# Kernel tuning notes

Hardware: AMD Instinct MI355X
Metric: run time of the kernel (lower is better)

The kernel has to match this reference:

```python
import jax, jax.numpy as jnp
import numpy as np

DIM_TIME = 100
NUM_HEAD = 8
DIM_OUT = 256
LN_EPS = 1e-5

# fixed (non-trainable) TimeEncode frequencies: 1 / 10**linspace(0, 9, dim)
_TIME_W = jnp.asarray((1.0 / 10 ** np.linspace(0, 9, DIM_TIME, dtype=np.float32)))


def setup_inputs() -> dict:
    key = jax.random.key(0)
    ks = jax.random.split(key, 16)
    D, E, S = 25000, 500000, 525000
    dn, de = 128, 128
    def lin(k, out_d, in_d):
        return jax.random.normal(k, (out_d, in_d), jnp.float32) * (1.0 / np.sqrt(in_d))
    return {
        "h": jax.random.normal(ks[0], (S, dn), jnp.float32),
        "f": jax.random.normal(ks[1], (E, de), jnp.float32),
        "dt": jax.random.uniform(ks[2], (E,), jnp.float32) * 1000.0,
        "Wq_lin": lin(ks[3], DIM_OUT, dn + DIM_TIME),
        "bq_lin": jnp.zeros((DIM_OUT,), jnp.float32),
        "Wkv_lin": lin(ks[4], DIM_OUT, dn + de + DIM_TIME),
        "bkv_lin": jnp.zeros((DIM_OUT,), jnp.float32),
        "Wq": lin(ks[5], DIM_OUT, DIM_OUT),
        "bq": jnp.zeros((DIM_OUT,), jnp.float32),
        "Wk": lin(ks[6], DIM_OUT, DIM_OUT),
        "bk": jnp.zeros((DIM_OUT,), jnp.float32),
        "Wv": lin(ks[7], DIM_OUT, DIM_OUT),
        "bv": jnp.zeros((DIM_OUT,), jnp.float32),
        "ln_g": jnp.ones((DIM_OUT,), jnp.float32),
        "ln_b": jnp.zeros((DIM_OUT,), jnp.float32),
        "dst": jax.random.randint(ks[8], (E,), 0, D, jnp.int64 if jax.config.jax_enable_x64 else jnp.int32),
    }


def reference(h, f, dt, Wq_lin, bq_lin, Wkv_lin, bkv_lin, Wq, bq, Wk, bk, Wv, bv, ln_g, ln_b, dst):
    E = dst.shape[0]
    D = h.shape[0] - E          # num_dst_nodes; src node D+i is the source of edge i
    H = NUM_HEAD
    dh = DIM_OUT // H

    # TimeEncode (frozen, no grad in original): cos(w * t + 0)
    time_feat = jax.lax.stop_gradient(jnp.cos(dt[:, None] * _TIME_W[None, :]))      # [E, Dt]
    zero_time_feat = jnp.ones((D, DIM_TIME), h.dtype)                               # cos(0) = 1

    # Q from dst nodes; K/V from src-neighbor nodes + edge feat + time feat
    Q_ori = jnp.concatenate([h[:D], zero_time_feat], axis=1) @ Wq_lin.T + bq_lin    # [D, dout]
    K_ori = jnp.concatenate([h[D:], f, time_feat], axis=1) @ Wkv_lin.T + bkv_lin    # [E, dout]

    # augmented edge set: E real edges + D self-loops (dst attends to itself)
    Qfull = jnp.concatenate([Q_ori[dst], Q_ori], axis=0)                            # [E+D, dout]
    KVfull = jnp.concatenate([K_ori, Q_ori], axis=0)                                # [E+D, dout]

    Qh = (Qfull @ Wq.T + bq).reshape(-1, H, dh)
    Kh = (KVfull @ Wk.T + bk).reshape(-1, H, dh)
    Vh = (KVfull @ Wv.T + bv).reshape(-1, H, dh)

    scores = jax.nn.leaky_relu(jnp.sum(Qh * Kh, axis=2), negative_slope=0.2)        # [E+D, H]

    dst_all = jnp.concatenate([dst, jnp.arange(D, dtype=dst.dtype)], axis=0)        # [E+D]

    # segment (edge) softmax over destination nodes; every dst has a self-loop
    seg_max = jnp.full((D, H), -jnp.inf, scores.dtype).at[dst_all].max(scores)
    ex = jnp.exp(scores - seg_max[dst_all])
    seg_sum = jnp.zeros((D, H), scores.dtype).at[dst_all].add(ex)
    att = ex / seg_sum[dst_all]                                                     # [E+D, H]

    # weighted scatter-sum aggregation (copy_u/sum over the augmented block)
    Vw = (Vh * att[:, :, None]).reshape(-1, DIM_OUT)                                # [E+D, dout]
    agg = jnp.zeros((D, DIM_OUT), h.dtype).at[dst_all].add(Vw)                      # [D, dout]

    rst = jax.nn.relu(agg)                                                          # dropout = identity (eval)
    mu = jnp.mean(rst, axis=-1, keepdims=True)
    var = jnp.mean((rst - mu) ** 2, axis=-1, keepdims=True)
    return (rst - mu) * jax.lax.rsqrt(var + LN_EPS) * ln_g + ln_b
```

## Files before the change

kernel.cpp:

```cpp
#include <hip/hip_runtime.h>
#include <cstdint>
#include <cstddef>


typedef _Float16 f16_t;
typedef _Float16 f16x8 __attribute__((ext_vector_type(8)));
typedef _Float16 f16x4 __attribute__((ext_vector_type(4)));
typedef float    f32x4 __attribute__((ext_vector_type(4)));

#define MFMA16(a, b, c) __builtin_amdgcn_mfma_f32_16x16x32_f16(a, b, c, 0, 0, 0)

#define BARRIER()                                         \
  do {                                                    \
    asm volatile("s_waitcnt lgkmcnt(0)" ::: "memory");    \
    __builtin_amdgcn_sched_barrier(0);                    \
    __builtin_amdgcn_s_barrier();                         \
    __builtin_amdgcn_sched_barrier(0);                    \
  } while (0)

static __device__ __forceinline__ f32x4 zero4() {
  f32x4 v; v[0] = 0.f; v[1] = 0.f; v[2] = 0.f; v[3] = 0.f; return v;
}

#define TIMEW_LOG2 (-0.30199346317157837f)

__global__ void k_prep(const float* __restrict__ wq_lin,
                       const float* __restrict__ bq_lin,
                       const float* __restrict__ wq,
                       const float* __restrict__ wk,
                       const float* __restrict__ wv,
                       f16_t* __restrict__ wq1,
                       f16_t* __restrict__ w3,
                       float* __restrict__ bqe) {
  int i = blockIdx.x * 256 + threadIdx.x;
  if (i < 32768) {
    int o = i >> 7, k = i & 127;
    wq1[i] = (f16_t)wq_lin[o * 228 + k];
  } else if (i < 229376) {
    int j = i - 32768;
    int r = j >> 8, k = j & 255;
    const float* src = (r < 256) ? wq : ((r < 512) ? wk : wv);
    w3[j] = (f16_t)src[(r & 255) * 256 + k];
  } else if (i < 229632) {
    int o = i - 229376;
    float s = bq_lin[o];
    for (int j = 0; j < 100; ++j) s += wq_lin[o * 228 + 128 + j];
    bqe[o] = s;
  }
}

__global__ __launch_bounds__(384) void k_wcomp(
    const float* __restrict__ wkv_lin, const float* __restrict__ bkv,
    const float* __restrict__ wk, const float* __restrict__ bk,
    const float* __restrict__ wv, const float* __restrict__ bv,
    f16_t* __restrict__ weffp, float* __restrict__ beff) {
  __shared__ float wrow[256];
  const int oc = blockIdx.x;
  const float* src = (oc < 256) ? (wk + (size_t)oc * 256)
                                : (wv + (size_t)(oc - 256) * 256);
  const int t = threadIdx.x;
  if (t < 256) wrow[t] = src[t];
  __syncthreads();

  float acc = 0.f;
  if (t < 356) {
#pragma unroll 4
    for (int m = 0; m < 256; ++m) acc += wrow[m] * wkv_lin[(size_t)m * 356 + t];
  }
  int kc = t >> 5, g = (t >> 3) & 3, j = t & 7;
  weffp[(size_t)kc * 16384 + g * 4096 + oc * 8 + j] = (f16_t)acc;

  if (t == 0) {
    float b = (oc < 256) ? bk[oc] : bv[oc - 256];
    for (int m = 0; m < 256; ++m) b += wrow[m] * bkv[m];
    beff[oc] = b;
  }
}

__global__ void k_hist(const int* __restrict__ dst, int* __restrict__ rs, int E) {
  int e = blockIdx.x * 256 + threadIdx.x;
  if (e < E) atomicAdd(&rs[dst[e] + 1], 1);
}

__global__ void k_scan(int* __restrict__ rs, int* __restrict__ cur, int D) {
  __shared__ int sd[1024];
  __shared__ int srun;
  const int t = threadIdx.x;
  if (t == 0) srun = 0;
  __syncthreads();
  for (int base = 0; base < D; base += 1024) {
    const int i = base + t;
    int c = (i < D) ? rs[i + 1] : 0;
    sd[t] = c;
    __syncthreads();
    for (int off = 1; off < 1024; off <<= 1) {
      int v = (t >= off) ? sd[t - off] : 0;
      __syncthreads();
      sd[t] += v;
      __syncthreads();
    }
    const int incl = sd[t];
    const int run = srun;
    __syncthreads();
    if (i < D) {
      cur[i] = run + incl - c;
      rs[i + 1] = run + incl;
    }
    if (t == 1023) srun = run + sd[1023];
    __syncthreads();
  }
}

__global__ void k_scatter(const int* __restrict__ dst, int* __restrict__ cur,
                          int* __restrict__ csr, int* __restrict__ dstc, int E) {
  int e = blockIdx.x * 256 + threadIdx.x;
  if (e < E) {
    int d = dst[e];
    int pos = atomicAdd(&cur[d], 1);
    csr[pos] = e;
    dstc[pos] = d;
  }
}

__global__ void k_sentinel(float* __restrict__ o, int n) {
  int i = blockIdx.x * 256 + threadIdx.x;
  if (i < n) o[i] = 1e30f;
}

__global__ __launch_bounds__(512) void k_q(
    const float* __restrict__ h, const float* __restrict__ bqe,
    const float* __restrict__ bq, const float* __restrict__ bk,
    const float* __restrict__ bv, const f16_t* __restrict__ wq1,
    const f16_t* __restrict__ w3, float* __restrict__ qhd,
    f16_t* __restrict__ khs, f16_t* __restrict__ vhs, int D) {
  __shared__ f16_t sm[64 * 256];
  f16_t* xs = sm;
  f16_t* ks = sm;
  const int tid = threadIdx.x;
  const int dbase = blockIdx.x * 64;

  {
    const int r = tid >> 3, q = tid & 7;
    const int dd = min(dbase + r, D - 1);
    const int sw = r & 7;
    const float* p = h + (size_t)dd * 128 + q * 16;
#pragma unroll
    for (int u = 0; u < 2; ++u) {
      float4 v0 = *(const float4*)(p + u * 8);
      float4 v1 = *(const float4*)(p + u * 8 + 4);
      f16x8 w8;
      w8[0] = (f16_t)v0.x; w8[1] = (f16_t)v0.y; w8[2] = (f16_t)v0.z; w8[3] = (f16_t)v0.w;
      w8[4] = (f16_t)v1.x; w8[5] = (f16_t)v1.y; w8[6] = (f16_t)v1.z; w8[7] = (f16_t)v1.w;
      *(f16x8*)&xs[r * 128 + (((2 * q + u) ^ sw) << 3)] = w8;
    }
  }
  __syncthreads();

  const int lane = tid & 63;
  const int wv_ = tid >> 6;
  const int m16 = lane & 15;
  const int g = lane >> 4;

  f32x4 acc1[4][2];
#pragma unroll
  for (int mt = 0; mt < 4; ++mt)
#pragma unroll
    for (int nt = 0; nt < 2; ++nt) acc1[mt][nt] = zero4();

#pragma unroll
  for (int kt = 0; kt < 4; ++kt) {
    f16x8 a[4];
#pragma unroll
    for (int mt = 0; mt < 4; ++mt) {
      int row = mt * 16 + m16;
      a[mt] = *(const f16x8*)&xs[row * 128 + ((((kt << 2) + g) ^ (row & 7)) << 3)];
    }
#pragma unroll
    for (int nt = 0; nt < 2; ++nt) {
      int col = wv_ * 32 + nt * 16 + m16;
      f16x8 b = *(const f16x8*)&wq1[(size_t)col * 128 + (kt << 5) + (g << 3)];
#pragma unroll
      for (int mt = 0; mt < 4; ++mt) acc1[mt][nt] = MFMA16(a[mt], b, acc1[mt][nt]);
    }
  }
  __syncthreads();

#pragma unroll
  for (int nt = 0; nt < 2; ++nt) {
    int col = wv_ * 32 + nt * 16 + m16;
    float bias = bqe[col];
#pragma unroll
    for (int mt = 0; mt < 4; ++mt)
#pragma unroll
      for (int j = 0; j < 4; ++j) {
        int row = mt * 16 + (g << 2) + j;
        ks[row * 256 + ((((col >> 3) ^ (row & 7)) << 3)) + (col & 7)] =
            (f16_t)(acc1[mt][nt][j] + bias);
      }
  }
  __syncthreads();

#pragma unroll
  for (int p = 0; p < 3; ++p) {
    const f16_t* wsec = w3 + ((size_t)p << 16);
    const float* bsec = (p == 0) ? bq : ((p == 1) ? bk : bv);
    f32x4 acc[4][2];
#pragma unroll
    for (int mt = 0; mt < 4; ++mt)
#pragma unroll
      for (int nt = 0; nt < 2; ++nt) acc[mt][nt] = zero4();
#pragma unroll
    for (int kt = 0; kt < 8; ++kt) {
      f16x8 a[4];
#pragma unroll
      for (int mt = 0; mt < 4; ++mt) {
        int row = mt * 16 + m16;
        a[mt] = *(const f16x8*)&ks[row * 256 + ((((kt << 2) + g) ^ (row & 7)) << 3)];
      }
#pragma unroll
      for (int nt = 0; nt < 2; ++nt) {
        int col = wv_ * 32 + nt * 16 + m16;
        f16x8 b = *(const f16x8*)&wsec[(size_t)col * 256 + (kt << 5) + (g << 3)];
#pragma unroll
        for (int mt = 0; mt < 4; ++mt) acc[mt][nt] = MFMA16(a[mt], b, acc[mt][nt]);
      }
    }
#pragma unroll
    for (int nt = 0; nt < 2; ++nt) {
      int col = wv_ * 32 + nt * 16 + m16;
      float bias = bsec[col];
#pragma unroll
      for (int mt = 0; mt < 4; ++mt)
#pragma unroll
        for (int j = 0; j < 4; ++j) {
          int row = mt * 16 + (g << 2) + j;
          int dd = dbase + row;
          if (dd < D) {
            float val = acc[mt][nt][j] + bias;
            if (p == 0)
              qhd[(size_t)dd * 256 + col] = val;
            else if (p == 1)
              khs[(size_t)dd * 256 + col] = (f16_t)val;
            else
              vhs[(size_t)dd * 256 + col] = (f16_t)val;
          }
        }
    }
  }
}

__global__ __launch_bounds__(512, 4) void k_kv(
    const float* __restrict__ h, const float* __restrict__ f,
    const float* __restrict__ dt, const f16_t* __restrict__ weffp,
    const float* __restrict__ beff, const int* __restrict__ csr,
    const int* __restrict__ dstc, const float* __restrict__ qhd,
    float* __restrict__ att, f16_t* __restrict__ vhg, int D, int E) {
  __shared__ __align__(16) unsigned char smem[40960];

  const int tid = threadIdx.x;
  const int pbase = blockIdx.x * 64;
  const int row = tid >> 3, q = tid & 7;
  const int lane = tid & 63, wn = tid >> 6;
  const int m16 = lane & 15, g = lane >> 4;

  const int pclamp = min(pbase + row, E - 1);
  const int ec = csr[pclamp];
  const float dtv = dt[ec];
  const float* hrow = h + (size_t)(D + ec) * 128 + q * 4;
  const float* frow = f + (size_t)ec * 128 + q * 4;

  auto stageA = [&](int buf, int sub, float4 v) {
    f16x4 w;
    w[0] = (f16_t)v.x; w[1] = (f16_t)v.y; w[2] = (f16_t)v.z; w[3] = (f16_t)v.w;
    *(f16x4*)(smem + buf * 20480 + sub * 5120 + row * 80 + q * 8) = w;
  };
  const f16_t* wb = weffp + (size_t)g * 4096 + ((size_t)(wn * 64 + m16) << 3);
  auto gldB = [&](int kc, f16x8* d) {
    const f16_t* pB = wb + (size_t)kc * 16384;
#pragma unroll
    for (int n = 0; n < 4; ++n) d[n] = *(const f16x8*)(pB + n * 128);
  };

  f32x4 acc[4][4];
#pragma unroll
  for (int mt = 0; mt < 4; ++mt)
#pragma unroll
    for (int n = 0; n < 4; ++n) acc[mt][n] = zero4();

  auto doChunk = [&](int kc, const f16x8* bbuf) {
    const unsigned char* Ac =
        smem + (((kc >> 2) == 1) ? 20480 : 0) + (kc & 3) * 5120;
#pragma unroll
    for (int mt = 0; mt < 4; ++mt) {
      f16x8 afr = *(const f16x8*)(Ac + (mt * 16 + m16) * 80 + g * 16);
#pragma unroll
      for (int n = 0; n < 4; ++n) acc[mt][n] = MFMA16(afr, bbuf[n], acc[mt][n]);
    }
  };

  float4 hv[4], fv[4];
#pragma unroll
  for (int s = 0; s < 4; ++s) hv[s] = *(const float4*)(hrow + s * 32);
#pragma unroll
  for (int s = 0; s < 4; ++s) fv[s] = *(const float4*)(frow + s * 32);
#pragma unroll
  for (int s = 0; s < 4; ++s) stageA(0, s, hv[s]);
#pragma unroll
  for (int s = 0; s < 4; ++s) stageA(1, s, fv[s]);
  BARRIER();

  f16x8 bb0[4], bb1[4];
  gldB(0, bb0);
  gldB(1, bb1); doChunk(0, bb0);
  gldB(2, bb0); doChunk(1, bb1);
  gldB(3, bb1); doChunk(2, bb0);
  gldB(4, bb0); doChunk(3, bb1);
  BARRIER();

#pragma unroll
  for (int s = 0; s < 4; ++s) {
    float4 a;
#pragma unroll
    for (int j = 0; j < 4; ++j) {
      int cc = s * 32 + q * 4 + j;
      ((float*)&a)[j] =
          (cc < 100) ? __cosf(dtv * exp2f(TIMEW_LOG2 * (float)cc)) : 0.f;
    }
    stageA(0, s, a);
  }
  gldB(5, bb1); doChunk(4, bb0);
  gldB(6, bb0); doChunk(5, bb1);
  gldB(7, bb1); doChunk(6, bb0);
  gldB(8, bb0); doChunk(7, bb1);
  BARRIER();

  gldB(9, bb1);  doChunk(8, bb0);
  gldB(10, bb0); doChunk(9, bb1);
  gldB(11, bb1); doChunk(10, bb0);
  doChunk(11, bb1);
  BARRIER();

  f16_t* ep = (f16_t*)smem;

  if (wn < 4) {
#pragma unroll
    for (int n = 0; n < 4; ++n) {
      const int c256 = wn * 64 + n * 16 + m16;
      const float bias = beff[c256];
#pragma unroll
      for (int mt = 0; mt < 4; ++mt)
#pragma unroll
        for (int j = 0; j < 4; ++j) {
          const int r2 = mt * 16 + (g << 2) + j;
          ep[r2 * 264 + c256] = (f16_t)(acc[mt][n][j] + bias);
        }
    }
  }
  BARRIER();

  {
    const int r2 = tid >> 3, hp = tid & 7;
    const int p2 = pbase + r2;
    if (p2 < E) {
      const int de = dstc[p2];
      const float* qp = qhd + (size_t)de * 256 + hp * 32;
      const f16_t* kp = ep + r2 * 264 + hp * 32;
      float s = 0.f;
#pragma unroll
      for (int jj = 0; jj < 32; jj += 4) {
        float4 qv = *(const float4*)(qp + jj);
        f16x4 kv = *(const f16x4*)(kp + jj);
        s += qv.x * (float)kv[0] + qv.y * (float)kv[1] +
             qv.z * (float)kv[2] + qv.w * (float)kv[3];
      }
      s = (s > 0.f) ? s : 0.2f * s;
      att[(size_t)p2 * 8 + hp] = __expf(s);
    }
  }
  BARRIER();

  if (wn >= 4) {
#pragma unroll
    for (int n = 0; n < 4; ++n) {
      const int c256 = (wn - 4) * 64 + n * 16 + m16;
      const float bias = beff[256 + c256];
#pragma unroll
      for (int mt = 0; mt < 4; ++mt)
#pragma unroll
        for (int j = 0; j < 4; ++j) {
          const int r2 = mt * 16 + (g << 2) + j;
          ep[r2 * 264 + c256] = (f16_t)(acc[mt][n][j] + bias);
        }
    }
  }
  BARRIER();

#pragma unroll
  for (int sweep = 0; sweep < 4; ++sweep) {
    const int flat = sweep * 4096 + tid * 8;
    const int r2 = flat >> 8, cc = flat & 255;
    const int p2 = pbase + r2;
    if (p2 < E) {
      f16x8 v = *(const f16x8*)&ep[r2 * 264 + cc];
      *(f16x8*)&vhg[(size_t)p2 * 256 + cc] = v;
    }
  }
}

__global__ __launch_bounds__(256) void k_agg(
    const float* __restrict__ qhd, const f16_t* __restrict__ khs,
    const f16_t* __restrict__ vhs, const float* __restrict__ att,
    const f16_t* __restrict__ vhg, const int* __restrict__ rs,
    const float* __restrict__ lng, const float* __restrict__ lnb,
    float* __restrict__ out, int D) {
  const int lane = threadIdx.x & 63;
  const int d = blockIdx.x * 4 + (threadIdx.x >> 6);
  if (d >= D) return;
  const int c0 = lane * 4;
  const int hd = lane >> 3;

  float den, a0, a1, a2, a3;
  {
    float4 qv = *(const float4*)(qhd + (size_t)d * 256 + c0);
    f16x4 ku = *(const f16x4*)(khs + (size_t)d * 256 + c0);
    f16x4 vu = *(const f16x4*)(vhs + (size_t)d * 256 + c0);
    float s = qv.x * (float)ku[0] + qv.y * (float)ku[1] +
              qv.z * (float)ku[2] + qv.w * (float)ku[3];
    s += __shfl_xor(s, 1); s += __shfl_xor(s, 2); s += __shfl_xor(s, 4);
    s = (s > 0.f) ? s : 0.2f * s;
    float ee = __expf(s);
    den = ee;
    a0 = ee * (float)vu[0]; a1 = ee * (float)vu[1];
    a2 = ee * (float)vu[2]; a3 = ee * (float)vu[3];
  }

  const int beg = rs[d], end = rs[d + 1];
  float ea0 = 0.f, ea1 = 0.f, ea2 = 0.f, ea3 = 0.f;
  float eb0 = 0.f, eb1 = 0.f, eb2 = 0.f, eb3 = 0.f;
  f16x4 va0 = {}, va1 = {}, va2 = {}, va3 = {};
  f16x4 vb0 = {}, vb1 = {}, vb2 = {}, vb3 = {};

#define LDQ(i, ee, vv)                                          \
  if ((i) < end) {                                              \
    ee = att[(size_t)(i) * 8 + hd];                             \
    vv = *(const f16x4*)(vhg + (size_t)(i) * 256 + c0);         \
  }
#define ACC(ee, vv)                                             \
  do {                                                          \
    den += ee;                                                  \
    a0 = fmaf(ee, (float)vv[0], a0);                            \
    a1 = fmaf(ee, (float)vv[1], a1);                            \
    a2 = fmaf(ee, (float)vv[2], a2);                            \
    a3 = fmaf(ee, (float)vv[3], a3);                            \
  } while (0)

  LDQ(beg + 0, ea0, va0);
  LDQ(beg + 1, ea1, va1);
  LDQ(beg + 2, ea2, va2);
  LDQ(beg + 3, ea3, va3);
  for (int idx = beg; idx < end; idx += 4) {
    LDQ(idx + 4, eb0, vb0);
    LDQ(idx + 5, eb1, vb1);
    LDQ(idx + 6, eb2, vb2);
    LDQ(idx + 7, eb3, vb3);
    ACC(ea0, va0);
    if (idx + 1 < end) ACC(ea1, va1);
    if (idx + 2 < end) ACC(ea2, va2);
    if (idx + 3 < end) ACC(ea3, va3);
    ea0 = eb0; va0 = vb0;
    ea1 = eb1; va1 = vb1;
    ea2 = eb2; va2 = vb2;
    ea3 = eb3; va3 = vb3;
  }
#undef LDQ
#undef ACC

  float x0 = fmaxf(a0 / den, 0.f), x1 = fmaxf(a1 / den, 0.f);
  float x2 = fmaxf(a2 / den, 0.f), x3 = fmaxf(a3 / den, 0.f);

  float s1 = x0 + x1 + x2 + x3;
#pragma unroll
  for (int m = 1; m < 64; m <<= 1) s1 += __shfl_xor(s1, m);
  float mu = s1 * (1.f / 256.f);
  float d0 = x0 - mu, d1 = x1 - mu, d2 = x2 - mu, d3 = x3 - mu;
  float s2 = d0 * d0 + d1 * d1 + d2 * d2 + d3 * d3;
#pragma unroll
  for (int m = 1; m < 64; m <<= 1) s2 += __shfl_xor(s2, m);
  float rstd = rsqrtf(s2 * (1.f / 256.f) + 1e-5f);

  float4 gg = *(const float4*)(lng + c0);
  float4 bb = *(const float4*)(lnb + c0);
  float4 o;
  o.x = d0 * rstd * gg.x + bb.x;
  o.y = d1 * rstd * gg.y + bb.y;
  o.z = d2 * rstd * gg.z + bb.z;
  o.w = d3 * rstd * gg.w + bb.w;
  *(float4*)(out + (size_t)d * 256 + c0) = o;
}

extern "C" void kernel_launch(void* const* d_in, const int* in_sizes, int n_in,
                              void* d_out, int out_size, void* d_ws,
                              size_t ws_size, hipStream_t stream) {
  const float* h       = (const float*)d_in[0];
  const float* f       = (const float*)d_in[1];
  const float* dt      = (const float*)d_in[2];
  const float* wq_lin  = (const float*)d_in[3];
  const float* bq_lin  = (const float*)d_in[4];
  const float* wkv_lin = (const float*)d_in[5];
  const float* bkv_lin = (const float*)d_in[6];
  const float* wq      = (const float*)d_in[7];
  const float* bq      = (const float*)d_in[8];
  const float* wk      = (const float*)d_in[9];
  const float* bk      = (const float*)d_in[10];
  const float* wv      = (const float*)d_in[11];
  const float* bv      = (const float*)d_in[12];
  const float* lng     = (const float*)d_in[13];
  const float* lnb     = (const float*)d_in[14];
  const int*   dst     = (const int*)d_in[15];

  const int S = in_sizes[0] / 128;
  const int E = in_sizes[2];
  const int D = S - E;
  float* out = (float*)d_out;

  char* p = (char*)d_ws;
  size_t off = 0;
  auto take = [&](size_t bytes) -> char* {
    char* r = p + off;
    off += (bytes + 255) & ~(size_t)255;
    return r;
  };
  f16_t* wq1   = (f16_t*)take((size_t)32768 * 2);
  f16_t* w3    = (f16_t*)take((size_t)196608 * 2);
  float* bqe   = (float*)take((size_t)256 * 4);
  f16_t* weffp = (f16_t*)take((size_t)196608 * 2);
  float* beff  = (float*)take((size_t)512 * 4);
  float* qhd   = (float*)take((size_t)D * 256 * 4);
  f16_t* khs   = (f16_t*)take((size_t)D * 256 * 2);
  f16_t* vhs   = (f16_t*)take((size_t)D * 256 * 2);
  float* att   = (float*)take((size_t)E * 8 * 4);
  f16_t* vhg   = (f16_t*)take((size_t)E * 256 * 2);
  int*   rs    = (int*)  take((size_t)(D + 1) * 4);
  int*   cur   = (int*)  take((size_t)D * 4);
  int*   csr   = (int*)  take((size_t)E * 4);
  int*   dstc  = (int*)  take((size_t)E * 4);

  if (off > ws_size) {
    k_sentinel<<<(out_size + 255) / 256, 256, 0, stream>>>(out, out_size);
    return;
  }

  hipMemsetAsync(rs, 0, (size_t)(D + 1) * 4, stream);
  k_prep<<<898, 256, 0, stream>>>(wq_lin, bq_lin, wq, wk, wv, wq1, w3, bqe);
  k_wcomp<<<512, 384, 0, stream>>>(wkv_lin, bkv_lin, wk, bk, wv, bv, weffp,
                                   beff);
  k_hist<<<(E + 255) / 256, 256, 0, stream>>>(dst, rs, E);
  k_scan<<<1, 1024, 0, stream>>>(rs, cur, D);
  k_scatter<<<(E + 255) / 256, 256, 0, stream>>>(dst, cur, csr, dstc, E);
  k_q<<<(D + 63) / 64, 512, 0, stream>>>(h, bqe, bq, bk, bv, wq1, w3, qhd, khs,
                                         vhs, D);
  k_kv<<<(E + 63) / 64, 512, 0, stream>>>(h, f, dt, weffp, beff, csr, dstc,
                                          qhd, att, vhg, D, E);
  k_agg<<<(D + 3) / 4, 256, 0, stream>>>(qhd, khs, vhs, att, vhg, rs, lng, lnb,
                                         out, D);
}
```

Baseline: 593.0 us.

## Fuse edge aggregation into k_kv via in-block segmented atomic accumulation

```diff
diff --git a/kernel.cpp b/kernel.cpp
--- a/kernel.cpp
+++ b/kernel.cpp
@@ -254,7 +254,7 @@
     const float* __restrict__ dt, const f16_t* __restrict__ weffp,
     const float* __restrict__ beff, const int* __restrict__ csr,
     const int* __restrict__ dstc, const float* __restrict__ qhd,
-    float* __restrict__ att, f16_t* __restrict__ vhg, int D, int E) {
+    float* __restrict__ agg, int D, int E) {
   __shared__ __align__(16) unsigned char smem[40960];
 
   const int tid = threadIdx.x;
@@ -340,7 +340,9 @@
   doChunk(11, bb1);
   BARRIER();
 
-  f16_t* ep = (f16_t*)smem;
+  f16_t* ep    = (f16_t*)smem;
+  float* ee_s  = (float*)(smem + 33792);
+  int*   dst_s = (int*)(smem + 35840);
 
   if (wn < 4) {
 #pragma unroll
@@ -361,6 +363,7 @@
   {
     const int r2 = tid >> 3, hp = tid & 7;
     const int p2 = pbase + r2;
+    float eev = 0.f;
     if (p2 < E) {
       const int de = dstc[p2];
       const float* qp = qhd + (size_t)de * 256 + hp * 32;
@@ -374,8 +377,10 @@
              qv.z * (float)kv[2] + qv.w * (float)kv[3];
       }
       s = (s > 0.f) ? s : 0.2f * s;
-      att[(size_t)p2 * 8 + hp] = __expf(s);
-    }
+      eev = __expf(s);
+    }
+    ee_s[r2 * 8 + hp] = eev;
+    if (hp == 0) dst_s[r2] = dstc[min(p2, E - 1)];
   }
   BARRIER();
 
@@ -395,22 +400,32 @@
   }
   BARRIER();
 
-#pragma unroll
-  for (int sweep = 0; sweep < 4; ++sweep) {
-    const int flat = sweep * 4096 + tid * 8;
-    const int r2 = flat >> 8, cc = flat & 255;
-    const int p2 = pbase + r2;
-    if (p2 < E) {
-      f16x8 v = *(const f16x8*)&ep[r2 * 264 + cc];
-      *(f16x8*)&vhg[(size_t)p2 * 256 + cc] = v;
-    }
-  }
-}
-
-__global__ __launch_bounds__(256) void k_agg(
+  if (tid < 264) {
+    const int c = tid;
+    const int hd = (c < 256) ? (c >> 5) : (c - 256);
+    float accv = 0.f;
+    int cur_d = dst_s[0];
+#pragma unroll 8
+    for (int r = 0; r < 64; ++r) {
+      int dd = dst_s[r];
+      if (dd != cur_d) {
+        atomicAdd(&agg[(size_t)cur_d * 264 + c], accv);
+        accv = 0.f;
+        cur_d = dd;
+      }
+      float eev = ee_s[r * 8 + hd];
+      if (c < 256)
+        accv = fmaf(eev, (float)ep[r * 264 + c], accv);
+      else
+        accv += eev;
+    }
+    atomicAdd(&agg[(size_t)cur_d * 264 + c], accv);
+  }
+}
+
+__global__ __launch_bounds__(256) void k_fin(
     const float* __restrict__ qhd, const f16_t* __restrict__ khs,
-    const f16_t* __restrict__ vhs, const float* __restrict__ att,
-    const f16_t* __restrict__ vhg, const int* __restrict__ rs,
+    const f16_t* __restrict__ vhs, const float* __restrict__ agg,
     const float* __restrict__ lng, const float* __restrict__ lnb,
     float* __restrict__ out, int D) {
   const int lane = threadIdx.x & 63;
@@ -419,7 +434,9 @@
   const int c0 = lane * 4;
   const int hd = lane >> 3;
 
-  float den, a0, a1, a2, a3;
+  float4 av = *(const float4*)(agg + (size_t)d * 264 + c0);
+  float den = agg[(size_t)d * 264 + 256 + hd];
+
   {
     float4 qv = *(const float4*)(qhd + (size_t)d * 256 + c0);
     f16x4 ku = *(const f16x4*)(khs + (size_t)d * 256 + c0);
@@ -429,54 +446,15 @@
     s += __shfl_xor(s, 1); s += __shfl_xor(s, 2); s += __shfl_xor(s, 4);
     s = (s > 0.f) ? s : 0.2f * s;
     float ee = __expf(s);
-    den = ee;
-    a0 = ee * (float)vu[0]; a1 = ee * (float)vu[1];
-    a2 = ee * (float)vu[2]; a3 = ee * (float)vu[3];
-  }
-
-  const int beg = rs[d], end = rs[d + 1];
-  float ea0 = 0.f, ea1 = 0.f, ea2 = 0.f, ea3 = 0.f;
-  float eb0 = 0.f, eb1 = 0.f, eb2 = 0.f, eb3 = 0.f;
-  f16x4 va0 = {}, va1 = {}, va2 = {}, va3 = {};
-  f16x4 vb0 = {}, vb1 = {}, vb2 = {}, vb3 = {};
-
-#define LDQ(i, ee, vv)                                          \
-  if ((i) < end) {                                              \
-    ee = att[(size_t)(i) * 8 + hd];                             \
-    vv = *(const f16x4*)(vhg + (size_t)(i) * 256 + c0);         \
-  }
-#define ACC(ee, vv)                                             \
-  do {                                                          \
-    den += ee;                                                  \
-    a0 = fmaf(ee, (float)vv[0], a0);                            \
-    a1 = fmaf(ee, (float)vv[1], a1);                            \
-    a2 = fmaf(ee, (float)vv[2], a2);                            \
-    a3 = fmaf(ee, (float)vv[3], a3);                            \
-  } while (0)
-
-  LDQ(beg + 0, ea0, va0);
-  LDQ(beg + 1, ea1, va1);
-  LDQ(beg + 2, ea2, va2);
-  LDQ(beg + 3, ea3, va3);
-  for (int idx = beg; idx < end; idx += 4) {
-    LDQ(idx + 4, eb0, vb0);
-    LDQ(idx + 5, eb1, vb1);
-    LDQ(idx + 6, eb2, vb2);
-    LDQ(idx + 7, eb3, vb3);
-    ACC(ea0, va0);
-    if (idx + 1 < end) ACC(ea1, va1);
-    if (idx + 2 < end) ACC(ea2, va2);
-    if (idx + 3 < end) ACC(ea3, va3);
-    ea0 = eb0; va0 = vb0;
-    ea1 = eb1; va1 = vb1;
-    ea2 = eb2; va2 = vb2;
-    ea3 = eb3; va3 = vb3;
-  }
-#undef LDQ
-#undef ACC
-
-  float x0 = fmaxf(a0 / den, 0.f), x1 = fmaxf(a1 / den, 0.f);
-  float x2 = fmaxf(a2 / den, 0.f), x3 = fmaxf(a3 / den, 0.f);
+    den += ee;
+    av.x = fmaf(ee, (float)vu[0], av.x);
+    av.y = fmaf(ee, (float)vu[1], av.y);
+    av.z = fmaf(ee, (float)vu[2], av.z);
+    av.w = fmaf(ee, (float)vu[3], av.w);
+  }
+
+  float x0 = fmaxf(av.x / den, 0.f), x1 = fmaxf(av.y / den, 0.f);
+  float x2 = fmaxf(av.z / den, 0.f), x3 = fmaxf(av.w / den, 0.f);
 
   float s1 = x0 + x1 + x2 + x3;
 #pragma unroll
@@ -538,8 +516,7 @@
   float* qhd   = (float*)take((size_t)D * 256 * 4);
   f16_t* khs   = (f16_t*)take((size_t)D * 256 * 2);
   f16_t* vhs   = (f16_t*)take((size_t)D * 256 * 2);
-  float* att   = (float*)take((size_t)E * 8 * 4);
-  f16_t* vhg   = (f16_t*)take((size_t)E * 256 * 2);
+  float* agg   = (float*)take((size_t)D * 264 * 4);
   int*   rs    = (int*)  take((size_t)(D + 1) * 4);
   int*   cur   = (int*)  take((size_t)D * 4);
   int*   csr   = (int*)  take((size_t)E * 4);
@@ -551,6 +528,7 @@
   }
 
   hipMemsetAsync(rs, 0, (size_t)(D + 1) * 4, stream);
+  hipMemsetAsync(agg, 0, (size_t)D * 264 * 4, stream);
   k_prep<<<898, 256, 0, stream>>>(wq_lin, bq_lin, wq, wk, wv, wq1, w3, bqe);
   k_wcomp<<<512, 384, 0, stream>>>(wkv_lin, bkv_lin, wk, bk, wv, bv, weffp,
                                    beff);
@@ -560,7 +538,6 @@
   k_q<<<(D + 63) / 64, 512, 0, stream>>>(h, bqe, bq, bk, bv, wq1, w3, qhd, khs,
                                          vhs, D);
   k_kv<<<(E + 63) / 64, 512, 0, stream>>>(h, f, dt, weffp, beff, csr, dstc,
-                                          qhd, att, vhg, D, E);
-  k_agg<<<(D + 3) / 4, 256, 0, stream>>>(qhd, khs, vhs, att, vhg, rs, lng, lnb,
-                                         out, D);
-}
+                                          qhd, agg, D, E);
+  k_fin<<<(D + 3) / 4, 256, 0, stream>>>(qhd, khs, vhs, agg, lng, lnb, out, D);
+}
```

New measurement: 596.9 us. No clear change (+0.7%).
